# Optimization experiments

Hardware: AMD Instinct MI355X
Metric: run time of the kernel (lower is better)

## Reference

```python
import jax, jax.numpy as jnp
import numpy as np

DIM = 256
H = 4
D = DIM // H  # head_dim = 64
SCALE = D ** -0.5


def setup_inputs() -> dict:
    key = jax.random.key(0)
    ks = jax.random.split(key, 12)
    B, N, M = 4, 2048, 2048
    x_query = jax.random.normal(ks[0], (B, N, DIM), dtype=jnp.float32)
    x_context = jax.random.normal(ks[1], (B, M, DIM), dtype=jnp.float32)
    geo_bias = jax.random.normal(ks[2], (B, H, N, M), dtype=jnp.float32)
    init = 1.0 / np.sqrt(DIM)
    Wq = jax.random.uniform(ks[3], (DIM, DIM), jnp.float32, -init, init)
    bq = jax.random.uniform(ks[4], (DIM,), jnp.float32, -init, init)
    Wk = jax.random.uniform(ks[5], (DIM, DIM), jnp.float32, -init, init)
    bk = jax.random.uniform(ks[6], (DIM,), jnp.float32, -init, init)
    Wv = jax.random.uniform(ks[7], (DIM, DIM), jnp.float32, -init, init)
    bv = jax.random.uniform(ks[8], (DIM,), jnp.float32, -init, init)
    Wo = jax.random.uniform(ks[9], (DIM, DIM), jnp.float32, -init, init)
    bo = jax.random.uniform(ks[10], (DIM,), jnp.float32, -init, init)
    return {"x_query": x_query, "x_context": x_context, "geo_bias": geo_bias,
            "Wq": Wq, "bq": bq, "Wk": Wk, "bk": bk, "Wv": Wv, "bv": bv,
            "Wo": Wo, "bo": bo}


def reference(x_query, x_context, geo_bias, Wq, bq, Wk, bk, Wv, bv, Wo, bo):
    B, N, _ = x_query.shape
    M = x_context.shape[1]
    # projections; nn.Linear computes x @ W.T + b
    q = (x_query @ Wq.T + bq).reshape(B, N, H, D).transpose(0, 2, 1, 3)   # (B,H,N,D)
    k = (x_context @ Wk.T + bk).reshape(B, M, H, D).transpose(0, 2, 1, 3)  # (B,H,M,D)
    v = (x_context @ Wv.T + bv).reshape(B, M, H, D).transpose(0, 2, 1, 3)  # (B,H,M,D)
    attn = jnp.einsum("bhnd,bhmd->bhnm", q, k) * SCALE + geo_bias
    attn = jax.nn.softmax(attn, axis=-1)
    out = jnp.einsum("bhnm,bhmd->bhnd", attn, v)
    out = out.transpose(0, 2, 1, 3).reshape(B, N, DIM)
    return out @ Wo.T + bo
```

## Files before the change

### kernel.cpp

```cpp
#include <hip/hip_runtime.h>

typedef unsigned short u16;
typedef unsigned int u32;
using bf16x8  = __attribute__((ext_vector_type(8))) __bf16;
using u16x8   = __attribute__((ext_vector_type(8), may_alias)) u16;
using u16x4   = __attribute__((ext_vector_type(4), may_alias)) u16;
using f32x4   = __attribute__((ext_vector_type(4))) float;
using f32x4_a = __attribute__((ext_vector_type(4), may_alias)) float;

#define DEV __device__ __forceinline__

constexpr int Bn = 4, Hn = 4, Nn = 2048, Mn = 2048, Dn = 64, DIMn = 256;
constexpr float SCALEc = 0.125f;
constexpr float SHIFTc = 12.0f;
constexpr int LSTRIDE = 76;

DEV float bf2f(u16 h) { u32 u = ((u32)h) << 16; return __builtin_bit_cast(float, u); }
DEV u16 f2bf(float f) {
    u32 u = __builtin_bit_cast(u32, f);
    u += 0x7fffu + ((u >> 16) & 1u);
    return (u16)(u >> 16);
}
DEV bf16x8 ld8bf(const u16* p) {
    return __builtin_bit_cast(bf16x8, *reinterpret_cast<const u16x8*>(p));
}
DEV bf16x8 ld8f_bf(const float* p) {
    const f32x4 a = *reinterpret_cast<const f32x4_a*>(p);
    const f32x4 b = *reinterpret_cast<const f32x4_a*>(p + 4);
    u16x8 r;
    r[0] = f2bf(a[0]); r[1] = f2bf(a[1]); r[2] = f2bf(a[2]); r[3] = f2bf(a[3]);
    r[4] = f2bf(b[0]); r[5] = f2bf(b[1]); r[6] = f2bf(b[2]); r[7] = f2bf(b[3]);
    return __builtin_bit_cast(bf16x8, r);
}

typedef __attribute__((address_space(1))) const unsigned int as1_uint;
typedef __attribute__((address_space(3))) unsigned int as3_uint;
DEV void dma16(const float* g, float* l) {
    __builtin_amdgcn_global_load_lds((as1_uint*)g, (as3_uint*)l, 16, 0, 0);
}

__global__ __launch_bounds__(256) void qkv_kernel(
    const float* __restrict__ Xq, const float* __restrict__ Wq, const float* __restrict__ bq,
    const float* __restrict__ Xc, const float* __restrict__ Wk, const float* __restrict__ bk,
    const float* __restrict__ Wv, const float* __restrict__ bv,
    float* __restrict__ Q, u16* __restrict__ K, u16* __restrict__ V)
{
    const int wave = threadIdx.x >> 6, lane = threadIdx.x & 63;
    const int quad = lane >> 4, l16 = lane & 15;
    const int o0 = wave * 64;

    if (blockIdx.x < 512) {
        const int row0 = blockIdx.x * 16;
        const int b = row0 >> 11, n0 = row0 & 2047;
        f32x4 acc[4] = {};
        #pragma unroll
        for (int k0 = 0; k0 < 256; k0 += 32) {
            const bf16x8 af = ld8f_bf(Xq + (size_t)(row0 + l16) * DIMn + k0 + quad * 8);
            #pragma unroll
            for (int os = 0; os < 4; os++) {
                const bf16x8 wf = ld8f_bf(Wq + (size_t)(o0 + os * 16 + l16) * DIMn + k0 + quad * 8);
                acc[os] = __builtin_amdgcn_mfma_f32_16x16x32_bf16(af, wf, acc[os], 0, 0, 0);
            }
        }
        #pragma unroll
        for (int os = 0; os < 4; os++) {
            const int col = o0 + os * 16 + l16;
            const int h = col >> 6, d = col & 63;
            const float bb = bq[col];
            #pragma unroll
            for (int r = 0; r < 4; r++) {
                const int n = n0 + quad * 4 + r;
                Q[((size_t)(b * Hn + h) * Nn + n) * Dn + d] = acc[os][r] + bb;
            }
        }
    } else {
        const int row0 = (blockIdx.x - 512) * 16;
        const int b = row0 >> 11, n0 = row0 & 2047;
        f32x4 ack[4] = {};
        f32x4 acv[4] = {};
        #pragma unroll
        for (int k0 = 0; k0 < 256; k0 += 32) {
            const bf16x8 af = ld8f_bf(Xc + (size_t)(row0 + l16) * DIMn + k0 + quad * 8);
            #pragma unroll
            for (int os = 0; os < 4; os++) {
                const bf16x8 wkf = ld8f_bf(Wk + (size_t)(o0 + os * 16 + l16) * DIMn + k0 + quad * 8);
                ack[os] = __builtin_amdgcn_mfma_f32_16x16x32_bf16(af, wkf, ack[os], 0, 0, 0);
                const bf16x8 wvf = ld8f_bf(Wv + (size_t)(o0 + os * 16 + l16) * DIMn + k0 + quad * 8);
                acv[os] = __builtin_amdgcn_mfma_f32_16x16x32_bf16(wvf, af, acv[os], 0, 0, 0);
            }
        }
        #pragma unroll
        for (int os = 0; os < 4; os++) {
            const int col = o0 + os * 16 + l16;
            const int h = col >> 6, d = col & 63;
            const float bb = bk[col];
            #pragma unroll
            for (int r = 0; r < 4; r++) {
                const int m = n0 + quad * 4 + r;
                K[((size_t)(b * Hn + h) * Mn + m) * Dn + d] = f2bf(ack[os][r] + bb);
            }
        }
        #pragma unroll
        for (int os = 0; os < 4; os++)
            #pragma unroll
            for (int r = 0; r < 4; r++) {
                const int colf = o0 + os * 16 + quad * 4 + r;
                const int h = colf >> 6, d = colf & 63;
                const float bb = bv[colf];
                const int m = n0 + l16;
                V[((size_t)(b * Hn + h) * Dn + d) * Mn + m] = f2bf(acv[os][r] + bb);
            }
    }
}

__global__ __launch_bounds__(64) void attn_kernel(
    const float* __restrict__ Q,
    const u16* __restrict__ K,
    const u16* __restrict__ V,
    const float* __restrict__ geo,
    float* __restrict__ Pnum,
    float* __restrict__ Lsum,
    int S)
{
    __shared__ __align__(16) u16 plds[16 * LSTRIDE];
    __shared__ __align__(16) float glds[2][4][256];

    const int h = blockIdx.y;
    const int b = blockIdx.z / S, split = blockIdx.z % S;
    const int lane = threadIdx.x & 63;
    const int quad = lane >> 4, l16 = lane & 15;
    const int nbase = blockIdx.x * 16;
    const int mlen = Mn / S, mbeg = split * mlen, mend = mbeg + mlen;

    const float* Qh = Q + ((size_t)(b * Hn + h) * Nn + nbase) * Dn;
    const u16*   Kh = K + (size_t)(b * Hn + h) * Mn * Dn;
    const u16*   Vh = V + (size_t)(b * Hn + h) * Dn * Mn;
    const float* Gl = geo + ((size_t)(b * Hn + h) * Nn + nbase + l16) * (size_t)Mn + quad * 4;

    bf16x8 qh[2], ql[2];
    #pragma unroll
    for (int kh = 0; kh < 2; kh++) {
        const float* qp = Qh + (size_t)l16 * Dn + kh * 32 + quad * 8;
        const f32x4 a = *reinterpret_cast<const f32x4_a*>(qp);
        const f32x4 c = *reinterpret_cast<const f32x4_a*>(qp + 4);
        u16x8 hi, lo;
        #pragma unroll
        for (int j = 0; j < 4; j++) {
            hi[j] = f2bf(a[j]); lo[j] = f2bf(a[j] - bf2f(hi[j]));
            hi[4 + j] = f2bf(c[j]); lo[4 + j] = f2bf(c[j] - bf2f(hi[4 + j]));
        }
        qh[kh] = __builtin_bit_cast(bf16x8, hi);
        ql[kh] = __builtin_bit_cast(bf16x8, lo);
    }

    f32x4 oacc[4] = {};
    float lsum = 0.f;
    const u16* kbase = Kh + (size_t)l16 * Dn + quad * 8;
    const u16* vbase = Vh + (size_t)l16 * Mn + quad * 8;

    #pragma unroll
    for (int ms = 0; ms < 4; ms++)
        dma16(Gl + mbeg + ms * 16, &glds[0][ms][0]);
    #pragma unroll
    for (int ms = 0; ms < 4; ms++)
        dma16(Gl + mbeg + 64 + ms * 16, &glds[1][ms][0]);
    bf16x8 kb0 = ld8bf(kbase + (size_t)mbeg * Dn);
    bf16x8 kb1 = ld8bf(kbase + (size_t)mbeg * Dn + 32);

    int buf = 0;
    for (int m0 = mbeg; m0 < mend; m0 += 64, buf ^= 1) {
        asm volatile("s_waitcnt vmcnt(6)" ::: "memory");
        const float* gr = &glds[buf][0][0] + lane * 4;
        #pragma unroll
        for (int ms = 0; ms < 4; ms++) {
            int mb = m0 + (ms + 1) * 16;
            if (mb > mend - 16) mb = mend - 16;
            const u16* kp = kbase + (size_t)mb * Dn;
            const bf16x8 nk0 = ld8bf(kp);
            const bf16x8 nk1 = ld8bf(kp + 32);
            f32x4 s = {};
            __builtin_amdgcn_s_setprio(1);
            s = __builtin_amdgcn_mfma_f32_16x16x32_bf16(kb0, qh[0], s, 0, 0, 0);
            s = __builtin_amdgcn_mfma_f32_16x16x32_bf16(kb0, ql[0], s, 0, 0, 0);
            s = __builtin_amdgcn_mfma_f32_16x16x32_bf16(kb1, qh[1], s, 0, 0, 0);
            s = __builtin_amdgcn_mfma_f32_16x16x32_bf16(kb1, ql[1], s, 0, 0, 0);
            __builtin_amdgcn_s_setprio(0);
            const f32x4 g = *reinterpret_cast<const f32x4_a*>(gr + ms * 256);
            u16x4 pk;
            float ls = 0.f;
            #pragma unroll
            for (int r = 0; r < 4; r++) {
                const float p = __expf(fmaf(s[r], SCALEc, g[r]) - SHIFTc);
                ls += p;
                pk[r] = f2bf(p);
            }
            lsum += ls;
            *reinterpret_cast<u16x4*>(plds + l16 * LSTRIDE + ms * 16 + quad * 4) = pk;
            kb0 = nk0; kb1 = nk1;
        }
        #pragma unroll
        for (int kh = 0; kh < 2; kh++) {
            const bf16x8 pa = ld8bf(plds + l16 * LSTRIDE + kh * 32 + quad * 8);
            bf16x8 vb[4];
            #pragma unroll
            for (int ds = 0; ds < 4; ds++)
                vb[ds] = ld8bf(vbase + (size_t)(ds * 16) * Mn + m0 + kh * 32);
            __builtin_amdgcn_s_setprio(1);
            #pragma unroll
            for (int ds = 0; ds < 4; ds++)
                oacc[ds] = __builtin_amdgcn_mfma_f32_16x16x32_bf16(pa, vb[ds], oacc[ds], 0, 0, 0);
            __builtin_amdgcn_s_setprio(0);
        }
        if (m0 + 128 < mend) {
            asm volatile("s_waitcnt lgkmcnt(0)" ::: "memory");
            #pragma unroll
            for (int ms = 0; ms < 4; ms++)
                dma16(Gl + (m0 + 128) + ms * 16, &glds[buf][ms][0]);
        }
    }

    lsum += __shfl_xor(lsum, 16);
    lsum += __shfl_xor(lsum, 32);

    float* PN = Pnum + (size_t)split * (Bn * (size_t)Nn * DIMn)
                     + ((size_t)b * Nn + nbase) * DIMn + h * Dn;
    #pragma unroll
    for (int r = 0; r < 4; r++)
        #pragma unroll
        for (int ds = 0; ds < 4; ds++)
            PN[(size_t)(quad * 4 + r) * DIMn + ds * 16 + l16] = oacc[ds][r];

    if (lane < 16)
        Lsum[(((size_t)split * Bn + b) * Hn + h) * Nn + nbase + l16] = lsum;
}

__global__ __launch_bounds__(256) void oproj_kernel(
    const float* __restrict__ Pnum, const float* __restrict__ Lsum,
    const float* __restrict__ W, const float* __restrict__ bias,
    float* __restrict__ out, int S)
{
    const int row0 = blockIdx.x * 16;
    const int wave = threadIdx.x >> 6, lane = threadIdx.x & 63;
    const int quad = lane >> 4, l16 = lane & 15;
    const int o0 = wave * 64;
    const size_t slab = (size_t)Bn * Nn * DIMn;

    const int arow = row0 + l16;
    const int b = arow >> 11, n = arow & 2047;
    float inv[4];
    #pragma unroll
    for (int hh = 0; hh < 4; hh++) {
        float l = 0.f;
        for (int s = 0; s < S; s++)
            l += Lsum[(((size_t)s * Bn + b) * Hn + hh) * Nn + n];
        inv[hh] = 1.0f / l;
    }

    f32x4 acc[4] = {};
    #pragma unroll
    for (int k0 = 0; k0 < 256; k0 += 32) {
        f32x4 a0 = {}, a1 = {};
        for (int s = 0; s < S; s++) {
            const float* p = Pnum + (size_t)s * slab + (size_t)arow * DIMn + k0 + quad * 8;
            a0 += *reinterpret_cast<const f32x4_a*>(p);
            a1 += *reinterpret_cast<const f32x4_a*>(p + 4);
        }
        const float iv = inv[(k0 + quad * 8) >> 6];
        u16x8 r;
        #pragma unroll
        for (int j = 0; j < 4; j++) {
            r[j]     = f2bf(a0[j] * iv);
            r[4 + j] = f2bf(a1[j] * iv);
        }
        const bf16x8 af = __builtin_bit_cast(bf16x8, r);
        #pragma unroll
        for (int os = 0; os < 4; os++) {
            const bf16x8 wf = ld8f_bf(W + (size_t)(o0 + os * 16 + l16) * DIMn + k0 + quad * 8);
            acc[os] = __builtin_amdgcn_mfma_f32_16x16x32_bf16(af, wf, acc[os], 0, 0, 0);
        }
    }
    #pragma unroll
    for (int os = 0; os < 4; os++) {
        const int col = o0 + os * 16 + l16;
        const float bb = bias[col];
        #pragma unroll
        for (int r = 0; r < 4; r++) {
            const int row = row0 + quad * 4 + r;
            out[(size_t)row * DIMn + col] = acc[os][r] + bb;
        }
    }
}

extern "C" void kernel_launch(void* const* d_in, const int* in_sizes, int n_in,
                              void* d_out, int out_size, void* d_ws, size_t ws_size,
                              hipStream_t stream) {
    const float* xq  = (const float*)d_in[0];
    const float* xc  = (const float*)d_in[1];
    const float* geo = (const float*)d_in[2];
    const float* Wq  = (const float*)d_in[3];
    const float* bq  = (const float*)d_in[4];
    const float* Wk  = (const float*)d_in[5];
    const float* bk  = (const float*)d_in[6];
    const float* Wv  = (const float*)d_in[7];
    const float* bv  = (const float*)d_in[8];
    const float* Wo  = (const float*)d_in[9];
    const float* bo  = (const float*)d_in[10];

    const int S = (ws_size >= (40ull << 20)) ? 2 : 1;

    char* ws = (char*)d_ws;
    float* Qw   = (float*)ws;
    u16*   Kw   = (u16*)(ws + (8ull << 20));
    u16*   Vw   = (u16*)(ws + (12ull << 20));
    float* Pnum = (float*)(ws + (20ull << 20));
    float* Lsum = (float*)(ws + (20ull << 20) + (size_t)S * (8ull << 20));

    qkv_kernel<<<1024, 256, 0, stream>>>(xq, Wq, bq, xc, Wk, bk, Wv, bv, Qw, Kw, Vw);
    attn_kernel<<<dim3(Nn / 16, Hn, Bn * S), 64, 0, stream>>>(Qw, Kw, Vw, geo, Pnum, Lsum, S);
    oproj_kernel<<<Bn * Nn / 16, 256, 0, stream>>>(Pnum, Lsum, Wo, bo, (float*)d_out, S);
}
```

Before: 576.1 us.

## Stage K/V tiles into LDS via async DMA and pre-convert weights to bf16

The attention kernel now double-buffers K and V tiles in XOR-swizzled LDS using global_load_lds DMA, alongside the geo bias. The old direct per-lane global loads of K and V are replaced by LDS reads. A new wprep kernel converts all four weight matrices to bf16 once per call, so the projection kernels load bf16 weights instead of converting fp32 on every load. This raises LDS use per block and adds a small extra launch, and launch_bounds(64,1) may change register allocation.

```diff
diff --git a/kernel.cpp b/kernel.cpp
--- a/kernel.cpp
+++ b/kernel.cpp
@@ -35,14 +35,31 @@
 
 typedef __attribute__((address_space(1))) const unsigned int as1_uint;
 typedef __attribute__((address_space(3))) unsigned int as3_uint;
-DEV void dma16(const float* g, float* l) {
+DEV void dma16(const void* g, void* l) {
     __builtin_amdgcn_global_load_lds((as1_uint*)g, (as3_uint*)l, 16, 0, 0);
 }
 
+__global__ __launch_bounds__(256) void wprep_kernel(
+    const float* __restrict__ Wq, const float* __restrict__ Wk,
+    const float* __restrict__ Wv, const float* __restrict__ Wo,
+    u16* __restrict__ Wb)
+{
+    const int idx = blockIdx.x * 256 + threadIdx.x;
+    const int m = idx >> 13;
+    const int off = (idx & 8191) * 8;
+    const float* src = (m == 0) ? Wq : (m == 1) ? Wk : (m == 2) ? Wv : Wo;
+    const f32x4 a = *reinterpret_cast<const f32x4_a*>(src + off);
+    const f32x4 c = *reinterpret_cast<const f32x4_a*>(src + off + 4);
+    u16x8 o;
+    #pragma unroll
+    for (int j = 0; j < 4; j++) { o[j] = f2bf(a[j]); o[4 + j] = f2bf(c[j]); }
+    *reinterpret_cast<u16x8*>(Wb + (size_t)m * 65536 + off) = o;
+}
+
 __global__ __launch_bounds__(256) void qkv_kernel(
-    const float* __restrict__ Xq, const float* __restrict__ Wq, const float* __restrict__ bq,
-    const float* __restrict__ Xc, const float* __restrict__ Wk, const float* __restrict__ bk,
-    const float* __restrict__ Wv, const float* __restrict__ bv,
+    const float* __restrict__ Xq, const u16* __restrict__ Wqb, const float* __restrict__ bq,
+    const float* __restrict__ Xc, const u16* __restrict__ Wkb, const float* __restrict__ bk,
+    const u16* __restrict__ Wvb, const float* __restrict__ bv,
     float* __restrict__ Q, u16* __restrict__ K, u16* __restrict__ V)
 {
     const int wave = threadIdx.x >> 6, lane = threadIdx.x & 63;
@@ -58,7 +75,7 @@
             const bf16x8 af = ld8f_bf(Xq + (size_t)(row0 + l16) * DIMn + k0 + quad * 8);
             #pragma unroll
             for (int os = 0; os < 4; os++) {
-                const bf16x8 wf = ld8f_bf(Wq + (size_t)(o0 + os * 16 + l16) * DIMn + k0 + quad * 8);
+                const bf16x8 wf = ld8bf(Wqb + (size_t)(o0 + os * 16 + l16) * DIMn + k0 + quad * 8);
                 acc[os] = __builtin_amdgcn_mfma_f32_16x16x32_bf16(af, wf, acc[os], 0, 0, 0);
             }
         }
@@ -83,9 +100,9 @@
             const bf16x8 af = ld8f_bf(Xc + (size_t)(row0 + l16) * DIMn + k0 + quad * 8);
             #pragma unroll
             for (int os = 0; os < 4; os++) {
-                const bf16x8 wkf = ld8f_bf(Wk + (size_t)(o0 + os * 16 + l16) * DIMn + k0 + quad * 8);
+                const bf16x8 wkf = ld8bf(Wkb + (size_t)(o0 + os * 16 + l16) * DIMn + k0 + quad * 8);
                 ack[os] = __builtin_amdgcn_mfma_f32_16x16x32_bf16(af, wkf, ack[os], 0, 0, 0);
-                const bf16x8 wvf = ld8f_bf(Wv + (size_t)(o0 + os * 16 + l16) * DIMn + k0 + quad * 8);
+                const bf16x8 wvf = ld8bf(Wvb + (size_t)(o0 + os * 16 + l16) * DIMn + k0 + quad * 8);
                 acv[os] = __builtin_amdgcn_mfma_f32_16x16x32_bf16(wvf, af, acv[os], 0, 0, 0);
             }
         }
@@ -113,7 +130,7 @@
     }
 }
 
-__global__ __launch_bounds__(64) void attn_kernel(
+__global__ __launch_bounds__(64, 1) void attn_kernel(
     const float* __restrict__ Q,
     const u16* __restrict__ K,
     const u16* __restrict__ V,
@@ -122,20 +139,27 @@
     float* __restrict__ Lsum,
     int S)
 {
-    __shared__ __align__(16) u16 plds[16 * LSTRIDE];
+    __shared__ __align__(16) u16   Klds[2][4096];
+    __shared__ __align__(16) u16   Vlds[2][4096];
     __shared__ __align__(16) float glds[2][4][256];
+    __shared__ __align__(16) u16   plds[16 * LSTRIDE];
 
     const int h = blockIdx.y;
     const int b = blockIdx.z / S, split = blockIdx.z % S;
     const int lane = threadIdx.x & 63;
     const int quad = lane >> 4, l16 = lane & 15;
+    const int r8 = lane >> 3, c8 = lane & 7;
+    const int swz = c8 ^ r8;
     const int nbase = blockIdx.x * 16;
-    const int mlen = Mn / S, mbeg = split * mlen, mend = mbeg + mlen;
+    const int mlen = Mn / S, mbeg = split * mlen;
+    const int nt = mlen / 64;
 
     const float* Qh = Q + ((size_t)(b * Hn + h) * Nn + nbase) * Dn;
     const u16*   Kh = K + (size_t)(b * Hn + h) * Mn * Dn;
     const u16*   Vh = V + (size_t)(b * Hn + h) * Dn * Mn;
-    const float* Gl = geo + ((size_t)(b * Hn + h) * Nn + nbase + l16) * (size_t)Mn + quad * 4;
+    const u16*   Ksrc = Kh + (size_t)r8 * Dn + swz * 8;
+    const u16*   Vsrc = Vh + (size_t)r8 * Mn + swz * 8;
+    const float* Gsrc = geo + ((size_t)(b * Hn + h) * Nn + nbase + l16) * (size_t)Mn + quad * 4;
 
     bf16x8 qh[2], ql[2];
     #pragma unroll
@@ -153,31 +177,43 @@
         ql[kh] = __builtin_bit_cast(bf16x8, lo);
     }
 
+    auto issue = [&](int m0n, int bq) {
+        float* gb = &glds[bq][0][0];
+        #pragma unroll
+        for (int ms = 0; ms < 4; ms++)
+            dma16(Gsrc + m0n + ms * 16, gb + ms * 256);
+        u16* kb = &Klds[bq][0];
+        #pragma unroll
+        for (int i = 0; i < 8; i++)
+            dma16(Ksrc + (size_t)m0n * Dn + i * 512, kb + i * 512);
+        u16* vbp = &Vlds[bq][0];
+        #pragma unroll
+        for (int i = 0; i < 8; i++)
+            dma16(Vsrc + m0n + (size_t)i * 8 * Mn, vbp + i * 512);
+    };
+
     f32x4 oacc[4] = {};
     float lsum = 0.f;
-    const u16* kbase = Kh + (size_t)l16 * Dn + quad * 8;
-    const u16* vbase = Vh + (size_t)l16 * Mn + quad * 8;
-
-    #pragma unroll
-    for (int ms = 0; ms < 4; ms++)
-        dma16(Gl + mbeg + ms * 16, &glds[0][ms][0]);
-    #pragma unroll
-    for (int ms = 0; ms < 4; ms++)
-        dma16(Gl + mbeg + 64 + ms * 16, &glds[1][ms][0]);
-    bf16x8 kb0 = ld8bf(kbase + (size_t)mbeg * Dn);
-    bf16x8 kb1 = ld8bf(kbase + (size_t)mbeg * Dn + 32);
-
-    int buf = 0;
-    for (int m0 = mbeg; m0 < mend; m0 += 64, buf ^= 1) {
-        asm volatile("s_waitcnt vmcnt(6)" ::: "memory");
+    const int lsw = l16 & 7;
+
+    issue(mbeg, 0);
+    issue(mbeg + 64, 1);
+
+    for (int t = 0; t < nt; t++) {
+        const int m0 = mbeg + t * 64;
+        const int buf = t & 1;
+        if (t + 1 < nt) asm volatile("s_waitcnt vmcnt(20)" ::: "memory");
+        else            asm volatile("s_waitcnt vmcnt(0)"  ::: "memory");
+
+        const u16* kr = &Klds[buf][0];
+        const u16* vr = &Vlds[buf][0];
         const float* gr = &glds[buf][0][0] + lane * 4;
+
         #pragma unroll
         for (int ms = 0; ms < 4; ms++) {
-            int mb = m0 + (ms + 1) * 16;
-            if (mb > mend - 16) mb = mend - 16;
-            const u16* kp = kbase + (size_t)mb * Dn;
-            const bf16x8 nk0 = ld8bf(kp);
-            const bf16x8 nk1 = ld8bf(kp + 32);
+            const int row = (ms * 16 + l16) * 64;
+            const bf16x8 kb0 = ld8bf(kr + row + ((quad ^ lsw) << 3));
+            const bf16x8 kb1 = ld8bf(kr + row + (((quad + 4) ^ lsw) << 3));
             f32x4 s = {};
             __builtin_amdgcn_s_setprio(1);
             s = __builtin_amdgcn_mfma_f32_16x16x32_bf16(kb0, qh[0], s, 0, 0, 0);
@@ -196,7 +232,6 @@
             }
             lsum += ls;
             *reinterpret_cast<u16x4*>(plds + l16 * LSTRIDE + ms * 16 + quad * 4) = pk;
-            kb0 = nk0; kb1 = nk1;
         }
         #pragma unroll
         for (int kh = 0; kh < 2; kh++) {
@@ -204,19 +239,14 @@
             bf16x8 vb[4];
             #pragma unroll
             for (int ds = 0; ds < 4; ds++)
-                vb[ds] = ld8bf(vbase + (size_t)(ds * 16) * Mn + m0 + kh * 32);
+                vb[ds] = ld8bf(vr + (ds * 16 + l16) * 64 + ((((kh << 2) + quad) ^ lsw) << 3));
             __builtin_amdgcn_s_setprio(1);
             #pragma unroll
             for (int ds = 0; ds < 4; ds++)
                 oacc[ds] = __builtin_amdgcn_mfma_f32_16x16x32_bf16(pa, vb[ds], oacc[ds], 0, 0, 0);
             __builtin_amdgcn_s_setprio(0);
         }
-        if (m0 + 128 < mend) {
-            asm volatile("s_waitcnt lgkmcnt(0)" ::: "memory");
-            #pragma unroll
-            for (int ms = 0; ms < 4; ms++)
-                dma16(Gl + (m0 + 128) + ms * 16, &glds[buf][ms][0]);
-        }
+        if (t + 2 < nt) issue(m0 + 128, buf);
     }
 
     lsum += __shfl_xor(lsum, 16);
@@ -236,7 +266,7 @@
 
 __global__ __launch_bounds__(256) void oproj_kernel(
     const float* __restrict__ Pnum, const float* __restrict__ Lsum,
-    const float* __restrict__ W, const float* __restrict__ bias,
+    const u16* __restrict__ Wob, const float* __restrict__ bias,
     float* __restrict__ out, int S)
 {
     const int row0 = blockIdx.x * 16;
@@ -275,7 +305,7 @@
         const bf16x8 af = __builtin_bit_cast(bf16x8, r);
         #pragma unroll
         for (int os = 0; os < 4; os++) {
-            const bf16x8 wf = ld8f_bf(W + (size_t)(o0 + os * 16 + l16) * DIMn + k0 + quad * 8);
+            const bf16x8 wf = ld8bf(Wob + (size_t)(o0 + os * 16 + l16) * DIMn + k0 + quad * 8);
             acc[os] = __builtin_amdgcn_mfma_f32_16x16x32_bf16(af, wf, acc[os], 0, 0, 0);
         }
     }
@@ -312,10 +342,13 @@
     float* Qw   = (float*)ws;
     u16*   Kw   = (u16*)(ws + (8ull << 20));
     u16*   Vw   = (u16*)(ws + (12ull << 20));
+    u16*   Wb   = (u16*)(ws + (16ull << 20));
     float* Pnum = (float*)(ws + (20ull << 20));
     float* Lsum = (float*)(ws + (20ull << 20) + (size_t)S * (8ull << 20));
 
-    qkv_kernel<<<1024, 256, 0, stream>>>(xq, Wq, bq, xc, Wk, bk, Wv, bv, Qw, Kw, Vw);
+    wprep_kernel<<<128, 256, 0, stream>>>(Wq, Wk, Wv, Wo, Wb);
+    qkv_kernel<<<1024, 256, 0, stream>>>(xq, Wb, bq, xc, Wb + 65536, bk,
+                                         Wb + 131072, bv, Qw, Kw, Vw);
     attn_kernel<<<dim3(Nn / 16, Hn, Bn * S), 64, 0, stream>>>(Qw, Kw, Vw, geo, Pnum, Lsum, S);
-    oproj_kernel<<<Bn * Nn / 16, 256, 0, stream>>>(Pnum, Lsum, Wo, bo, (float*)d_out, S);
-}
+    oproj_kernel<<<Bn * Nn / 16, 256, 0, stream>>>(Pnum, Lsum, Wb + 196608, bo, (float*)d_out, S);
+}
```

New measurement: 515.5 us. 10.5% less time.
